# Optimization experiments

Measured on AMD Instinct MI355X. Metric: run time of the kernel, lower is better.

Reference implementation:

```python
import jax, jax.numpy as jnp
import numpy as np

N_NODES = 50000
N_EDGES = 800000
IN_F, HID, OUT = 128, 128, 64


def setup_inputs() -> dict:
    key = jax.random.key(0)
    ks = jax.random.split(key, 12)
    sc = 0.05
    return {
        "features": jax.random.normal(ks[0], (N_NODES, IN_F), jnp.float32),
        "src": jax.random.randint(ks[1], (N_EDGES,), 0, N_NODES, jnp.int32),
        "dst": jax.random.randint(ks[2], (N_EDGES,), 0, N_NODES, jnp.int32),
        "Wself0": jax.random.normal(ks[3], (IN_F, HID), jnp.float32) * sc,
        "Wneigh0": jax.random.normal(ks[4], (IN_F, HID), jnp.float32) * sc,
        "b0": jnp.zeros((HID,), jnp.float32),
        "Wself1": jax.random.normal(ks[5], (HID, HID), jnp.float32) * sc,
        "Wneigh1": jax.random.normal(ks[6], (HID, HID), jnp.float32) * sc,
        "b1": jnp.zeros((HID,), jnp.float32),
        "Wself2": jax.random.normal(ks[7], (HID, OUT), jnp.float32) * sc,
        "Wneigh2": jax.random.normal(ks[8], (HID, OUT), jnp.float32) * sc,
        "b2": jnp.zeros((OUT,), jnp.float32),
    }


def _sage_conv(h, src, dst, Ws, Wn, b, act):
    # mean aggregator: mean over in-neighbors (src -> dst), zero for isolated nodes
    msg = h[src]                                            # [E, d] gather
    agg = jax.ops.segment_sum(msg, dst, num_segments=N_NODES)
    deg = jax.ops.segment_sum(jnp.ones((msg.shape[0],), h.dtype), dst,
                              num_segments=N_NODES)
    mean = agg / jnp.maximum(deg, 1.0)[:, None]             # [N, d]
    out = h @ Ws + mean @ Wn + b                            # fc_self + fc_neigh + bias
    return jax.nn.relu(out) if act else out


def reference(features, src, dst, Wself0, Wneigh0, b0, Wself1, Wneigh1, b1,
              Wself2, Wneigh2, b2):
    h = _sage_conv(features, src, dst, Wself0, Wneigh0, b0, True)
    h = _sage_conv(h, src, dst, Wself1, Wneigh1, b1, True)
    h = _sage_conv(h, src, dst, Wself2, Wneigh2, b2, False)
    return h
```

## Files before the change

### kernel.cpp

```cpp
#include <hip/hip_runtime.h>
#include <hip/hip_fp16.h>

#define N_NODES_C 50000
#define N_EDGES_C 800000
#define K_FEAT 128
#define HM_STRIDE 256
#define NB_C 196

typedef unsigned int uint_t;
typedef signed char schar;
typedef schar schar8 __attribute__((ext_vector_type(8)));
typedef _Float16 half8 __attribute__((ext_vector_type(8)));
typedef _Float16 half4 __attribute__((ext_vector_type(4)));
typedef float f32x4 __attribute__((ext_vector_type(4)));


__global__ __launch_bounds__(256) void p1hist_conv_kernel(
    const int* __restrict__ dst, uint_t* __restrict__ histG, int E,
    const float* __restrict__ feat, _Float16* __restrict__ hm0,
    schar* __restrict__ q0, float* __restrict__ sc0,
    const float* __restrict__ Ws0, const float* __restrict__ Wn0,
    const float* __restrict__ Ws1, const float* __restrict__ Wn1,
    const float* __restrict__ Ws2, const float* __restrict__ Wn2,
    _Float16* __restrict__ WT0, _Float16* __restrict__ WT1, _Float16* __restrict__ WT2) {
    const int t = threadIdx.x, b = blockIdx.x;
    if (b < NB_C) {
        __shared__ uint_t hist[256];
        hist[t] = 0;
        __syncthreads();
        const int base = b * 4096;
#pragma unroll
        for (int j = 0; j < 16; ++j) {
            int idx = base + t + j * 256;
            if (idx < E) atomicAdd(&hist[((uint_t)dst[idx]) >> 8], 1u);
        }
        __syncthreads();
        histG[b * 256 + t] = hist[t];
    } else {
        const int i = (b - NB_C) * 256 + t;
        const int n4 = N_NODES_C * K_FEAT / 4;
        if (i < n4) {
            float4 v = reinterpret_cast<const float4*>(feat)[i];
            int n = i >> 5, c4 = i & 31;
            half4 o;
            o.x = (_Float16)v.x; o.y = (_Float16)v.y; o.z = (_Float16)v.z; o.w = (_Float16)v.w;
            *reinterpret_cast<half4*>(hm0 + (size_t)n * HM_STRIDE + c4 * 4) = o;
            float m = fmaxf(fmaxf(fabsf(v.x), fabsf(v.y)), fmaxf(fabsf(v.z), fabsf(v.w)));
            m = fmaxf(m, __shfl_xor(m, 1, 64));
            m = fmaxf(m, __shfl_xor(m, 2, 64));
            m = fmaxf(m, __shfl_xor(m, 4, 64));
            m = fmaxf(m, __shfl_xor(m, 8, 64));
            m = fmaxf(m, __shfl_xor(m, 16, 64));
            const float inv = (m > 0.f) ? 127.0f / m : 0.f;
            uint_t w = ((uint_t)(unsigned char)(schar)rintf(v.x * inv)) |
                       ((uint_t)(unsigned char)(schar)rintf(v.y * inv) << 8) |
                       ((uint_t)(unsigned char)(schar)rintf(v.z * inv) << 16) |
                       ((uint_t)(unsigned char)(schar)rintf(v.w * inv) << 24);
            *reinterpret_cast<uint_t*>(q0 + (size_t)n * 128 + c4 * 4) = w;
            if ((t & 31) == 0) sc0[n] = m * (1.0f / 127.0f);
        } else {
            int idx = i - n4;
            if (idx >= 81920) return;
            const float* Ws;
            const float* Wn;
            _Float16* WT;
            int ncol;
            if (idx < 32768) { Ws = Ws0; Wn = Wn0; WT = WT0; ncol = 128; }
            else if (idx < 65536) { idx -= 32768; Ws = Ws1; Wn = Wn1; WT = WT1; ncol = 128; }
            else { idx -= 65536; Ws = Ws2; Wn = Wn2; WT = WT2; ncol = 64; }
            int k = idx & 255, c = idx >> 8;
            float v = (k < 128) ? Ws[(size_t)k * ncol + c] : Wn[(size_t)(k - 128) * ncol + c];
            WT[(size_t)c * 256 + k] = (_Float16)v;
        }
    }
}

__global__ __launch_bounds__(256) void p1scan_kernel(uint_t* __restrict__ histG,
                                                     uint_t* __restrict__ cbase) {
    const int t = threadIdx.x;
    uint_t run = 0;
    for (int bb = 0; bb < NB_C; bb += 28) {
        uint_t vals[28];
#pragma unroll
        for (int j = 0; j < 28; ++j) vals[j] = histG[(size_t)(bb + j) * 256 + t];
#pragma unroll
        for (int j = 0; j < 28; ++j) {
            uint_t x = vals[j];
            vals[j] = run;
            run += x;
        }
#pragma unroll
        for (int j = 0; j < 28; ++j) histG[(size_t)(bb + j) * 256 + t] = vals[j];
    }
    const int lane = t & 63, wid = t >> 6;
    uint_t x = run;
#pragma unroll
    for (int off = 1; off < 64; off <<= 1) {
        uint_t y = __shfl_up(x, off, 64);
        if (lane >= off) x += y;
    }
    __shared__ uint_t wsum[4];
    if (lane == 63) wsum[wid] = x;
    __syncthreads();
    uint_t wpre = 0;
#pragma unroll
    for (int w = 0; w < 4; ++w)
        if (w < wid) wpre += wsum[w];
    uint_t incl = wpre + x;
    cbase[t] = incl - run;
    if (t == 255) cbase[256] = incl;
}

__global__ __launch_bounds__(256) void p1scatter_kernel(const int* __restrict__ src,
                                                        const int* __restrict__ dst,
                                                        const uint_t* __restrict__ histG,
                                                        const uint_t* __restrict__ cbase,
                                                        uint_t* __restrict__ tmp, int E) {
    __shared__ uint_t cur[256];
    const int t = threadIdx.x, b = blockIdx.x;
    cur[t] = histG[b * 256 + t] + cbase[t];
    __syncthreads();
    const int base = b * 4096;
#pragma unroll
    for (int j = 0; j < 16; ++j) {
        int idx = base + t + j * 256;
        if (idx < E) {
            uint_t d = (uint_t)dst[idx];
            uint_t s = (uint_t)src[idx];
            uint_t slot = atomicAdd(&cur[d >> 8], 1u);
            tmp[slot] = ((d & 255u) << 16) | s;
        }
    }
}

__global__ __launch_bounds__(256) void p2_kernel(const uint_t* __restrict__ tmp,
                                                 const uint_t* __restrict__ cbase,
                                                 int* __restrict__ offs, int* __restrict__ ssrc) {
    __shared__ uint_t hist[256];
    __shared__ uint_t cur[256];
    __shared__ uint_t wsum[4];
    const int t = threadIdx.x, c = blockIdx.x;
    const uint_t cb = cbase[c], ce = cbase[c + 1];
    hist[t] = 0;
    __syncthreads();
    for (uint_t i = cb + t; i < ce; i += 256) atomicAdd(&hist[tmp[i] >> 16], 1u);
    __syncthreads();
    const uint_t v = hist[t];
    const int lane = t & 63, wid = t >> 6;
    uint_t x = v;
#pragma unroll
    for (int off = 1; off < 64; off <<= 1) {
        uint_t y = __shfl_up(x, off, 64);
        if (lane >= off) x += y;
    }
    if (lane == 63) wsum[wid] = x;
    __syncthreads();
    uint_t wpre = 0;
#pragma unroll
    for (int w = 0; w < 4; ++w)
        if (w < wid) wpre += wsum[w];
    const uint_t excl = wpre + x - v;
    const int node = c * 256 + t;
    if (node < N_NODES_C) offs[node] = (int)(cb + excl);
    if (c == 0 && t == 0) offs[N_NODES_C] = N_EDGES_C;
    cur[t] = excl;
    __syncthreads();
    for (uint_t i = cb + t; i < ce; i += 256) {
        uint_t p = tmp[i];
        uint_t slot = cb + atomicAdd(&cur[p >> 16], 1u);
        ssrc[slot] = (int)(p & 0xFFFFu);
    }
}


__global__ void mean_kernel(const schar* __restrict__ q, const float* __restrict__ qsc,
                            _Float16* __restrict__ hm, const int* __restrict__ offs,
                            const int* __restrict__ ssrc) {
    const int node = (int)((blockIdx.x * blockDim.x + threadIdx.x) >> 6);
    const int lane = threadIdx.x & 63;
    if (node >= N_NODES_C) return;
    const int beg = offs[node], end = offs[node + 1];
    const int g = lane >> 4;
    const int cb = (lane & 15) * 8;
    const schar* base = q + cb;

    float accA[8] = {0.f, 0.f, 0.f, 0.f, 0.f, 0.f, 0.f, 0.f};
    float accB[8] = {0.f, 0.f, 0.f, 0.f, 0.f, 0.f, 0.f, 0.f};

    int e = beg;
    for (; e + 16 <= end; e += 16) {
        const int s0 = ssrc[e + g];
        const int s1 = ssrc[e + 4 + g];
        const int s2 = ssrc[e + 8 + g];
        const int s3 = ssrc[e + 12 + g];
        const float c0 = qsc[s0], c1 = qsc[s1], c2 = qsc[s2], c3 = qsc[s3];
        schar8 v0 = *reinterpret_cast<const schar8*>(base + (size_t)s0 * 128);
        schar8 v1 = *reinterpret_cast<const schar8*>(base + (size_t)s1 * 128);
        schar8 v2 = *reinterpret_cast<const schar8*>(base + (size_t)s2 * 128);
        schar8 v3 = *reinterpret_cast<const schar8*>(base + (size_t)s3 * 128);
#pragma unroll
        for (int j = 0; j < 8; ++j) accA[j] += c0 * (float)v0[j];
#pragma unroll
        for (int j = 0; j < 8; ++j) accB[j] += c1 * (float)v1[j];
#pragma unroll
        for (int j = 0; j < 8; ++j) accA[j] += c2 * (float)v2[j];
#pragma unroll
        for (int j = 0; j < 8; ++j) accB[j] += c3 * (float)v3[j];
    }
    for (; e + 8 <= end; e += 8) {
        const int s0 = ssrc[e + g];
        const int s1 = ssrc[e + 4 + g];
        const float c0 = qsc[s0], c1 = qsc[s1];
        schar8 v0 = *reinterpret_cast<const schar8*>(base + (size_t)s0 * 128);
        schar8 v1 = *reinterpret_cast<const schar8*>(base + (size_t)s1 * 128);
#pragma unroll
        for (int j = 0; j < 8; ++j) accA[j] += c0 * (float)v0[j];
#pragma unroll
        for (int j = 0; j < 8; ++j) accB[j] += c1 * (float)v1[j];
    }
    for (; e + 4 <= end; e += 4) {
        const int s0 = ssrc[e + g];
        const float c0 = qsc[s0];
        schar8 v0 = *reinterpret_cast<const schar8*>(base + (size_t)s0 * 128);
#pragma unroll
        for (int j = 0; j < 8; ++j) accA[j] += c0 * (float)v0[j];
    }
    if (e < end) {
        const bool valid = (e + g) < end;
        const int s0 = valid ? ssrc[e + g] : ssrc[beg];
        const float c0 = valid ? qsc[s0] : 0.f;
        schar8 v0 = *reinterpret_cast<const schar8*>(base + (size_t)s0 * 128);
#pragma unroll
        for (int j = 0; j < 8; ++j) accB[j] += c0 * (float)v0[j];
    }

    const float inv = (end > beg) ? 1.0f / (float)(end - beg) : 0.f;
    half8 o;
#pragma unroll
    for (int j = 0; j < 8; ++j) {
        float x = accA[j] + accB[j];
        x += __shfl_xor(x, 16, 64);
        x += __shfl_xor(x, 32, 64);
        o[j] = (_Float16)(x * inv);
    }
    if (lane < 16)
        *reinterpret_cast<half8*>(hm + (size_t)node * HM_STRIDE + 128 + cb) = o;
}


template <int NCOL, bool ACT, bool OUT_FP32>
__global__ __launch_bounds__(256) void sage_mfma(
    const _Float16* __restrict__ hm,
    const _Float16* __restrict__ WT,
    const float* __restrict__ bias,
    float* __restrict__ outf,
    _Float16* __restrict__ outh,
    schar* __restrict__ qout,
    float* __restrict__ scout,
    int nNodes) {
    constexpr int CF = NCOL / 16;
    constexpr int RPB = 128;

    __shared__ _Float16 bl[NCOL][256];

    const int t = threadIdx.x;
#pragma unroll
    for (int it = 0; it < NCOL * 32 / 256; ++it) {
        int f = t + it * 256;
        int row = f >> 5, c8 = f & 31;
        half8 v = *reinterpret_cast<const half8*>(WT + (size_t)row * 256 + c8 * 8);
        int col = (c8 * 8) ^ ((row & 7) << 3);
        *reinterpret_cast<half8*>(&bl[row][col]) = v;
    }
    __syncthreads();

    const int wid = t >> 6;
    const int lane = t & 63;
    const int r0 = blockIdx.x * RPB + wid * 32;
    const int koff = (lane >> 4) * 8;

    half8 a[2][8];
#pragma unroll
    for (int fr = 0; fr < 2; ++fr) {
        int row = r0 + fr * 16 + (lane & 15);
        if (row >= nNodes) row = nNodes - 1;
        const _Float16* ap = hm + (size_t)row * HM_STRIDE + koff;
#pragma unroll
        for (int ks = 0; ks < 8; ++ks)
            a[fr][ks] = *reinterpret_cast<const half8*>(ap + ks * 32);
    }

    f32x4 acc[2][CF];
#pragma unroll
    for (int fr = 0; fr < 2; ++fr)
#pragma unroll
        for (int c = 0; c < CF; ++c) acc[fr][c] = {0.f, 0.f, 0.f, 0.f};

#pragma unroll
    for (int c = 0; c < CF; ++c) {
        const int brow = c * 16 + (lane & 15);
        const int bswz = (brow & 7) << 3;
#pragma unroll
        for (int ks = 0; ks < 8; ++ks) {
            half8 b = *reinterpret_cast<const half8*>(&bl[brow][(ks * 32 + koff) ^ bswz]);
            acc[0][c] = __builtin_amdgcn_mfma_f32_16x16x32_f16(a[0][ks], b, acc[0][c], 0, 0, 0);
            acc[1][c] = __builtin_amdgcn_mfma_f32_16x16x32_f16(a[1][ks], b, acc[1][c], 0, 0, 0);
        }
    }

    const int ocol = lane & 15;
    const int orow_off = (lane >> 4) << 2;
    float bv[CF];
#pragma unroll
    for (int c = 0; c < CF; ++c) bv[c] = bias[c * 16 + ocol];

#pragma unroll
    for (int fr = 0; fr < 2; ++fr) {
#pragma unroll
        for (int reg = 0; reg < 4; ++reg) {
            const int row = r0 + fr * 16 + orow_off + reg;
            float vals[CF];
            float m = 0.f;
#pragma unroll
            for (int c = 0; c < CF; ++c) {
                float v = acc[fr][c][reg] + bv[c];
                if (ACT) v = fmaxf(v, 0.f);
                vals[c] = v;
                m = fmaxf(m, fabsf(v));
            }
            if (OUT_FP32) {
                if (row < nNodes) {
#pragma unroll
                    for (int c = 0; c < CF; ++c)
                        outf[(size_t)row * NCOL + c * 16 + ocol] = vals[c];
                }
            } else {
                m = fmaxf(m, __shfl_xor(m, 1, 64));
                m = fmaxf(m, __shfl_xor(m, 2, 64));
                m = fmaxf(m, __shfl_xor(m, 4, 64));
                m = fmaxf(m, __shfl_xor(m, 8, 64));
                const float qinv = (m > 0.f) ? 127.0f / m : 0.f;
                if (row < nNodes) {
#pragma unroll
                    for (int c = 0; c < CF; ++c) {
                        const int col = c * 16 + ocol;
                        outh[(size_t)row * HM_STRIDE + col] = (_Float16)vals[c];
                        qout[(size_t)row * 128 + col] = (schar)rintf(vals[c] * qinv);
                    }
                    if (ocol == 0) scout[row] = m * (1.0f / 127.0f);
                }
            }
        }
    }
}


extern "C" void kernel_launch(void* const* d_in, const int* in_sizes, int n_in,
                              void* d_out, int out_size, void* d_ws, size_t ws_size,
                              hipStream_t stream) {
    const float* feat = (const float*)d_in[0];
    const int* src = (const int*)d_in[1];
    const int* dst = (const int*)d_in[2];
    const float* Ws0 = (const float*)d_in[3];
    const float* Wn0 = (const float*)d_in[4];
    const float* b0 = (const float*)d_in[5];
    const float* Ws1 = (const float*)d_in[6];
    const float* Wn1 = (const float*)d_in[7];
    const float* b1 = (const float*)d_in[8];
    const float* Ws2 = (const float*)d_in[9];
    const float* Wn2 = (const float*)d_in[10];
    const float* b2 = (const float*)d_in[11];
    float* out = (float*)d_out;

    auto align_up = [](size_t x) { return (x + 255) & ~(size_t)255; };
    char* w = (char*)d_ws;
    uint_t* histG = (uint_t*)w; w += align_up((size_t)NB_C * 256 * 4);
    uint_t* cbase = (uint_t*)w; w += align_up(257 * 4);
    uint_t* tmp = (uint_t*)w;   w += align_up((size_t)N_EDGES_C * 4);
    int* offs = (int*)w;        w += align_up((size_t)(N_NODES_C + 1) * 4);
    int* ssrc = (int*)w;        w += align_up((size_t)N_EDGES_C * 4);
    _Float16* hm0 = (_Float16*)w; w += align_up((size_t)N_NODES_C * HM_STRIDE * 2);
    _Float16* hm1 = (_Float16*)w; w += align_up((size_t)N_NODES_C * HM_STRIDE * 2);
    schar* q0 = (schar*)w;      w += align_up((size_t)N_NODES_C * 128);
    schar* q1 = (schar*)w;      w += align_up((size_t)N_NODES_C * 128);
    float* sc0 = (float*)w;     w += align_up((size_t)N_NODES_C * 4);
    float* sc1 = (float*)w;     w += align_up((size_t)N_NODES_C * 4);
    _Float16* WT0 = (_Float16*)w; w += align_up((size_t)128 * 256 * 2);
    _Float16* WT1 = (_Float16*)w; w += align_up((size_t)128 * 256 * 2);
    _Float16* WT2 = (_Float16*)w; w += align_up((size_t)64 * 256 * 2);
    _Float16* hm2 = hm0;
    schar* q2 = q0;
    float* sc2 = sc0;

    const int convBlocks = (N_NODES_C * K_FEAT / 4 + 81920 + 255) / 256;
    p1hist_conv_kernel<<<NB_C + convBlocks, 256, 0, stream>>>(
        dst, histG, N_EDGES_C, feat, hm0, q0, sc0,
        Ws0, Wn0, Ws1, Wn1, Ws2, Wn2, WT0, WT1, WT2);
    p1scan_kernel<<<1, 256, 0, stream>>>(histG, cbase);
    p1scatter_kernel<<<NB_C, 256, 0, stream>>>(src, dst, histG, cbase, tmp, N_EDGES_C);
    p2_kernel<<<NB_C, 256, 0, stream>>>(tmp, cbase, offs, ssrc);

    const int meanBlocks = (N_NODES_C * 64 + 255) / 256;
    const int gemmBlocks = (N_NODES_C + 127) / 128;

    mean_kernel<<<meanBlocks, 256, 0, stream>>>(q0, sc0, hm0, offs, ssrc);
    sage_mfma<128, true, false><<<gemmBlocks, 256, 0, stream>>>(
        hm0, WT0, b0, nullptr, hm1, q1, sc1, N_NODES_C);

    mean_kernel<<<meanBlocks, 256, 0, stream>>>(q1, sc1, hm1, offs, ssrc);
    sage_mfma<128, true, false><<<gemmBlocks, 256, 0, stream>>>(
        hm1, WT1, b1, nullptr, hm2, q2, sc2, N_NODES_C);

    mean_kernel<<<meanBlocks, 256, 0, stream>>>(q2, sc2, hm2, offs, ssrc);
    sage_mfma<64, false, true><<<gemmBlocks, 256, 0, stream>>>(
        hm2, WT2, b2, out, nullptr, nullptr, nullptr, N_NODES_C);
}
```

Measured before the change: 154.9 us.

## Split quantized feature table into two column planes for two-pass gather

Stores int8 node features as two 64-column planes and runs the mean aggregation as two passes, one per plane. Each pass gathers from a half-size table, aiming for better L2 cache hit rates in the random neighbor gather. In exchange, CSR offsets and source indices are read twice, lanes cover 8 edges per step with a wider reduction, and the GEMM's quantized output writes are split across planes.

```diff
diff --git a/kernel.cpp b/kernel.cpp
--- a/kernel.cpp
+++ b/kernel.cpp
@@ -6,6 +6,7 @@
 #define K_FEAT 128
 #define HM_STRIDE 256
 #define NB_C 196
+#define MEAN_NB (N_NODES_C / 4)
 
 typedef unsigned int uint_t;
 typedef signed char schar;
@@ -13,6 +14,7 @@
 typedef _Float16 half8 __attribute__((ext_vector_type(8)));
 typedef _Float16 half4 __attribute__((ext_vector_type(4)));
 typedef float f32x4 __attribute__((ext_vector_type(4)));
+
 
 
 __global__ __launch_bounds__(256) void p1hist_conv_kernel(
@@ -56,7 +58,8 @@
                        ((uint_t)(unsigned char)(schar)rintf(v.y * inv) << 8) |
                        ((uint_t)(unsigned char)(schar)rintf(v.z * inv) << 16) |
                        ((uint_t)(unsigned char)(schar)rintf(v.w * inv) << 24);
-            *reinterpret_cast<uint_t*>(q0 + (size_t)n * 128 + c4 * 4) = w;
+            const int p = c4 >> 4, wc = (c4 & 15) * 4;
+            *reinterpret_cast<uint_t*>(q0 + ((size_t)p * N_NODES_C + n) * 64 + wc) = w;
             if ((t & 31) == 0) sc0[n] = m * (1.0f / 127.0f);
         } else {
             int idx = i - n4;
@@ -173,16 +176,20 @@
 }
 
 
-__global__ void mean_kernel(const schar* __restrict__ q, const float* __restrict__ qsc,
-                            _Float16* __restrict__ hm, const int* __restrict__ offs,
-                            const int* __restrict__ ssrc) {
-    const int node = (int)((blockIdx.x * blockDim.x + threadIdx.x) >> 6);
+__global__ __launch_bounds__(256) void mean_pass_kernel(const schar* __restrict__ q,
+                                                        const float* __restrict__ qsc,
+                                                        _Float16* __restrict__ hm,
+                                                        const int* __restrict__ offs,
+                                                        const int* __restrict__ ssrc) {
+    const int blk = blockIdx.x;
+    const int pass = blk / MEAN_NB;
+    const int nb = blk - pass * MEAN_NB;
+    const int node = nb * 4 + (threadIdx.x >> 6);
     const int lane = threadIdx.x & 63;
-    if (node >= N_NODES_C) return;
+    const int g = lane >> 3;
+    const int cb = (lane & 7) * 8;
+    const schar* base = q + (size_t)pass * N_NODES_C * 64 + cb;
     const int beg = offs[node], end = offs[node + 1];
-    const int g = lane >> 4;
-    const int cb = (lane & 15) * 8;
-    const schar* base = q + cb;
 
     float accA[8] = {0.f, 0.f, 0.f, 0.f, 0.f, 0.f, 0.f, 0.f};
     float accB[8] = {0.f, 0.f, 0.f, 0.f, 0.f, 0.f, 0.f, 0.f};
@@ -190,38 +197,19 @@
     int e = beg;
     for (; e + 16 <= end; e += 16) {
         const int s0 = ssrc[e + g];
-        const int s1 = ssrc[e + 4 + g];
-        const int s2 = ssrc[e + 8 + g];
-        const int s3 = ssrc[e + 12 + g];
-        const float c0 = qsc[s0], c1 = qsc[s1], c2 = qsc[s2], c3 = qsc[s3];
-        schar8 v0 = *reinterpret_cast<const schar8*>(base + (size_t)s0 * 128);
-        schar8 v1 = *reinterpret_cast<const schar8*>(base + (size_t)s1 * 128);
-        schar8 v2 = *reinterpret_cast<const schar8*>(base + (size_t)s2 * 128);
-        schar8 v3 = *reinterpret_cast<const schar8*>(base + (size_t)s3 * 128);
+        const int s1 = ssrc[e + 8 + g];
+        const float c0 = qsc[s0], c1 = qsc[s1];
+        schar8 v0 = *reinterpret_cast<const schar8*>(base + (size_t)s0 * 64);
+        schar8 v1 = *reinterpret_cast<const schar8*>(base + (size_t)s1 * 64);
 #pragma unroll
         for (int j = 0; j < 8; ++j) accA[j] += c0 * (float)v0[j];
 #pragma unroll
         for (int j = 0; j < 8; ++j) accB[j] += c1 * (float)v1[j];
-#pragma unroll
-        for (int j = 0; j < 8; ++j) accA[j] += c2 * (float)v2[j];
-#pragma unroll
-        for (int j = 0; j < 8; ++j) accB[j] += c3 * (float)v3[j];
     }
     for (; e + 8 <= end; e += 8) {
         const int s0 = ssrc[e + g];
-        const int s1 = ssrc[e + 4 + g];
-        const float c0 = qsc[s0], c1 = qsc[s1];
-        schar8 v0 = *reinterpret_cast<const schar8*>(base + (size_t)s0 * 128);
-        schar8 v1 = *reinterpret_cast<const schar8*>(base + (size_t)s1 * 128);
-#pragma unroll
-        for (int j = 0; j < 8; ++j) accA[j] += c0 * (float)v0[j];
-#pragma unroll
-        for (int j = 0; j < 8; ++j) accB[j] += c1 * (float)v1[j];
-    }
-    for (; e + 4 <= end; e += 4) {
-        const int s0 = ssrc[e + g];
         const float c0 = qsc[s0];
-        schar8 v0 = *reinterpret_cast<const schar8*>(base + (size_t)s0 * 128);
+        schar8 v0 = *reinterpret_cast<const schar8*>(base + (size_t)s0 * 64);
 #pragma unroll
         for (int j = 0; j < 8; ++j) accA[j] += c0 * (float)v0[j];
     }
@@ -229,7 +217,7 @@
         const bool valid = (e + g) < end;
         const int s0 = valid ? ssrc[e + g] : ssrc[beg];
         const float c0 = valid ? qsc[s0] : 0.f;
-        schar8 v0 = *reinterpret_cast<const schar8*>(base + (size_t)s0 * 128);
+        schar8 v0 = *reinterpret_cast<const schar8*>(base + (size_t)s0 * 64);
 #pragma unroll
         for (int j = 0; j < 8; ++j) accB[j] += c0 * (float)v0[j];
     }
@@ -239,12 +227,13 @@
 #pragma unroll
     for (int j = 0; j < 8; ++j) {
         float x = accA[j] + accB[j];
+        x += __shfl_xor(x, 8, 64);
         x += __shfl_xor(x, 16, 64);
         x += __shfl_xor(x, 32, 64);
         o[j] = (_Float16)(x * inv);
     }
-    if (lane < 16)
-        *reinterpret_cast<half8*>(hm + (size_t)node * HM_STRIDE + 128 + cb) = o;
+    if (lane < 8)
+        *reinterpret_cast<half8*>(hm + (size_t)node * HM_STRIDE + 128 + pass * 64 + cb) = o;
 }
 
 
@@ -345,7 +334,8 @@
                     for (int c = 0; c < CF; ++c) {
                         const int col = c * 16 + ocol;
                         outh[(size_t)row * HM_STRIDE + col] = (_Float16)vals[c];
-                        qout[(size_t)row * 128 + col] = (schar)rintf(vals[c] * qinv);
+                        qout[((size_t)(col >> 6) * N_NODES_C + row) * 64 + (col & 63)] =
+                            (schar)rintf(vals[c] * qinv);
                     }
                     if (ocol == 0) scout[row] = m * (1.0f / 127.0f);
                 }
@@ -400,18 +390,18 @@
     p1scatter_kernel<<<NB_C, 256, 0, stream>>>(src, dst, histG, cbase, tmp, N_EDGES_C);
     p2_kernel<<<NB_C, 256, 0, stream>>>(tmp, cbase, offs, ssrc);
 
-    const int meanBlocks = (N_NODES_C * 64 + 255) / 256;
+    const int meanBlocks = MEAN_NB * 2;
     const int gemmBlocks = (N_NODES_C + 127) / 128;
 
-    mean_kernel<<<meanBlocks, 256, 0, stream>>>(q0, sc0, hm0, offs, ssrc);
+    mean_pass_kernel<<<meanBlocks, 256, 0, stream>>>(q0, sc0, hm0, offs, ssrc);
     sage_mfma<128, true, false><<<gemmBlocks, 256, 0, stream>>>(
         hm0, WT0, b0, nullptr, hm1, q1, sc1, N_NODES_C);
 
-    mean_kernel<<<meanBlocks, 256, 0, stream>>>(q1, sc1, hm1, offs, ssrc);
+    mean_pass_kernel<<<meanBlocks, 256, 0, stream>>>(q1, sc1, hm1, offs, ssrc);
     sage_mfma<128, true, false><<<gemmBlocks, 256, 0, stream>>>(
         hm1, WT1, b1, nullptr, hm2, q2, sc2, N_NODES_C);
 
-    mean_kernel<<<meanBlocks, 256, 0, stream>>>(q2, sc2, hm2, offs, ssrc);
+    mean_pass_kernel<<<meanBlocks, 256, 0, stream>>>(q2, sc2, hm2, offs, ssrc);
     sage_mfma<64, false, true><<<gemmBlocks, 256, 0, stream>>>(
         hm2, WT2, b2, out, nullptr, nullptr, nullptr, N_NODES_C);
 }
```

Result: slower. 194.2 us (+25.4%).
